# Performance work log

Hardware: AMD Instinct MI355X
Metric: run time of the kernel (lower is better)

## Reference

```python
import jax, jax.numpy as jnp
import numpy as np

GROUPS = 16
KS = 3
EPS = 1e-5  # torch InstanceNorm2d default


def _leaky(x):
    return jnp.where(x > 0, x, 0.1 * x)


def setup_inputs() -> dict:
    key = jax.random.key(0)
    ks = jax.random.split(key, 9)
    B, C, H, W = 8, 256, 128, 128
    R = 512
    s = 0.05
    return {
        "x": jax.random.normal(ks[0], (B, C, H, W), jnp.float32),
        "representation": jax.random.normal(ks[1], (B, R), jnp.float32),
        # SConv.compress_key: Linear(R, C*3*3, bias=False)
        "w_key": jax.random.normal(ks[2], (C * KS * KS, R), jnp.float32) * s,
        # SRAdaIN gamma/beta Linears (R -> C, no bias)
        "w_gamma": jax.random.normal(ks[3], (C, R), jnp.float32) * s,
        "w_beta": jax.random.normal(ks[4], (C, R), jnp.float32) * s,
        # SCM: 1x1 convs R -> R/4 -> C (no bias), PReLU single param init 0.25
        "w_ca1": jax.random.normal(ks[5], (R // 4, R), jnp.float32) * s,
        "prelu_a": jnp.float32(0.25),
        "w_ca2": jax.random.normal(ks[6], (C, R // 4), jnp.float32) * s,
        # ConvLayer: 1x1 conv C -> C with bias
        "w_conv2": jax.random.normal(ks[7], (C, C), jnp.float32) * s,
        "b_conv2": jax.random.normal(ks[8], (C,), jnp.float32) * s,
    }


def reference(x, representation, w_key, w_gamma, w_beta, w_ca1, prelu_a, w_ca2, w_conv2, b_conv2):
    b, c_in, h, w = x.shape
    c_out = w_conv2.shape[0]
    fpg = c_in // GROUPS  # features per group

    # ---- SConv: per-sample dynamic grouped conv (reflection pad, valid conv) ----
    xp = jnp.pad(x, ((0, 0), (0, 0), (1, 1), (1, 1)), mode='reflect')
    # kernel: (b, c_out, 1, 3, 3) then repeat_interleave over in-per-group dim
    kern = _leaky(representation @ w_key.T).reshape(b, c_out, 1, KS, KS)
    kern = jnp.broadcast_to(kern, (b, c_out, fpg, KS, KS))

    def one_conv(xi, ki):
        # xi: (c_in, h+2, w+2); ki: (c_out, fpg, 3, 3)
        return jax.lax.conv_general_dilated(
            xi[None], ki, (1, 1), 'VALID',
            feature_group_count=GROUPS,
            dimension_numbers=('NCHW', 'OIHW', 'NCHW'))[0]

    out = jax.vmap(one_conv)(xp, kern)  # (b, c_out, h, w)

    # ---- SRAdaIN: instance norm (biased var) + learned affine from rep ----
    mean = out.mean(axis=(2, 3), keepdims=True)
    var = out.var(axis=(2, 3), keepdims=True)
    gamma = _leaky(representation @ w_gamma.T)[:, :, None, None]
    beta = _leaky(representation @ w_beta.T)[:, :, None, None]
    out = (out - mean) * jax.lax.rsqrt(var + EPS) * gamma + beta
    out = jax.nn.relu(out)

    # ---- SCM: channel attention gating of the residual ----
    hmid = representation @ w_ca1.T
    hmid = jnp.where(hmid > 0, hmid, prelu_a * hmid)  # PReLU
    att = jax.nn.sigmoid(hmid @ w_ca2.T)[:, :, None, None]  # (b, c_out, 1, 1)
    out = out + x * att

    # ---- ConvLayer: 1x1 conv with bias (pad=0) ----
    out = jnp.einsum('bchw,oc->bohw', out, w_conv2) + b_conv2[None, :, None, None]
    return out
```

## Files before the change

### kernel.cpp

```cpp
#include <hip/hip_runtime.h>
#include <hip/hip_bf16.h>

#define NB 8
#define NC 256
#define NH 128
#define NW 128
#define NR 512
#define NGROUPS 16
#define HP 130
#define NPIX (NH*NW)

#define OFF_KERN  0
#define OFF_GAMMA 18432
#define OFF_BETA  20480
#define OFF_ATT   22528
#define OFF_A     24576
#define OFF_B2    26624
#define OFF_HMID  28672
#define OFF_P     29696
#define OFF_GP    94208
#define OFF_APACK 2257408
#define OFF_PART  2322944

typedef __attribute__((ext_vector_type(8))) short bf16x8;
typedef __attribute__((ext_vector_type(4))) float f32x4;

__device__ __forceinline__ float leakyf(float v) { return v > 0.f ? v : 0.1f * v; }

__device__ __forceinline__ unsigned short f2bf(float f) {
    unsigned u = __float_as_uint(f);
    unsigned r = (u + 0x7FFFu + ((u >> 16) & 1u)) >> 16;
    return (unsigned short)r;
}
__device__ __forceinline__ float bf2f(unsigned short s) {
    return __uint_as_float(((unsigned)s) << 16);
}

__global__ __launch_bounds__(256) void k_params(
    const float* __restrict__ rep, const float* __restrict__ w_key,
    const float* __restrict__ w_gamma, const float* __restrict__ w_beta,
    const float* __restrict__ w_ca1, const float* __restrict__ prelu_a,
    float* __restrict__ ws)
{
    __shared__ float rep_s[NR];
    const int b = blockIdx.y, t = threadIdx.x;
    rep_s[t]       = rep[b*NR + t];
    rep_s[t + 256] = rep[b*NR + t + 256];
    __syncthreads();

    const int r = blockIdx.x * 64 + (t >> 2);
    const int part = t & 3;
    const float* wrow;
    if (r < 2304)      wrow = w_key   + (size_t)r * NR;
    else if (r < 2560) wrow = w_gamma + (size_t)(r - 2304) * NR;
    else if (r < 2816) wrow = w_beta  + (size_t)(r - 2560) * NR;
    else               wrow = w_ca1   + (size_t)(r - 2816) * NR;

    const float4* w4 = (const float4*)wrow + part*32;
    const float4* r4 = (const float4*)rep_s + part*32;
    float acc = 0.f;
    #pragma unroll
    for (int i = 0; i < 32; i++) {
        float4 a = r4[i], w = w4[i];
        acc += a.x*w.x + a.y*w.y + a.z*w.z + a.w*w.w;
    }
    acc += __shfl_xor(acc, 1, 64);
    acc += __shfl_xor(acc, 2, 64);

    if (part == 0) {
        if (r < 2816) {
            const float v = leakyf(acc);
            if (r < 2304)      ws[OFF_KERN  + b*NC*9 + r]        = v;
            else if (r < 2560) ws[OFF_GAMMA + b*NC + r - 2304]   = v;
            else               ws[OFF_BETA  + b*NC + r - 2560]   = v;
        } else {
            const float pa = prelu_a[0];
            ws[OFF_HMID + b*128 + r - 2816] = acc > 0.f ? acc : pa * acc;
        }
    }
}

__global__ __launch_bounds__(256) void k_pack(
    const float* __restrict__ W, float* __restrict__ ws)
{
    const int idx = blockIdx.x * 256 + threadIdx.x;
    const int j    = idx & 7;
    const int lane = (idx >> 3) & 63;
    const int mt   = (idx >> 9) & 15;
    const int ks   = idx >> 13;
    const int m = mt*16 + (lane & 15);
    const int k = ks*32 + (lane >> 4)*8 + j;
    unsigned short* ap = (unsigned short*)(ws + OFF_APACK);
    ap[((ks*16 + mt)*64 + lane)*8 + j] = f2bf(W[m*NC + k]);
}

__global__ __launch_bounds__(256) void k_gsum(
    const float* __restrict__ x, float* __restrict__ ws)
{
    const int t = threadIdx.x;
    const int l = t & 31;
    const int r = t >> 5;
    const int bid = blockIdx.x;
    const int rg = bid % 17;
    const int bg = bid / 17;
    const int yy = rg*8 + r;
    if (yy >= HP) return;
    int sy = yy - 1; if (sy < 0) sy = -sy; if (sy > NH-1) sy = 2*(NH-1) - sy;
    const float* xbase = x + (size_t)bg * 16 * NPIX + (size_t)sy * NW + l*4;
    float4 s = make_float4(0.f, 0.f, 0.f, 0.f);
    #pragma unroll
    for (int k = 0; k < 16; k++) {
        const float4 v = *(const float4*)(xbase + (size_t)k * NPIX);
        s.x += v.x; s.y += v.y; s.z += v.z; s.w += v.w;
    }
    float* gp = ws + OFF_GP + ((size_t)bg * HP + yy) * HP;
    gp[1 + l*4] = s.x;
    gp[2 + l*4] = s.y;
    gp[3 + l*4] = s.z;
    gp[4 + l*4] = s.w;
    if (l == 0)  gp[0]   = s.y;
    if (l == 31) gp[129] = s.z;
}

__global__ __launch_bounds__(256) void k_stats(float* __restrict__ ws)
{
    const int g = blockIdx.x, b = blockIdx.y, chunk = blockIdx.z, t = threadIdx.x;
    __shared__ float kern_s[16*9];
    __shared__ float red[256*32];
    if (t < 144) kern_s[t] = ws[OFF_KERN + (b*NC + g*16)*9 + t];
    __syncthreads();

    float s[16], q[16];
    #pragma unroll
    for (int i = 0; i < 16; i++) { s[i] = 0.f; q[i] = 0.f; }

    const float* gp = ws + OFF_GP + (size_t)(b*16 + g) * HP * HP;
    const int p0b = chunk * 4096;
    for (int pi = 0; pi < 16; pi++) {
        const int p = p0b + pi*256 + t;
        const int y = p >> 7, xc = p & 127;
        const float* pa = gp + y*HP + xc;
        const float p0 = pa[0],    p1 = pa[1],      p2 = pa[2];
        const float p3 = pa[HP],   p4 = pa[HP+1],   p5 = pa[HP+2];
        const float p6 = pa[2*HP], p7 = pa[2*HP+1], p8 = pa[2*HP+2];
        #pragma unroll
        for (int ch = 0; ch < 16; ch++) {
            const float* k9 = kern_s + ch*9;
            float v = k9[0]*p0 + k9[1]*p1 + k9[2]*p2
                    + k9[3]*p3 + k9[4]*p4 + k9[5]*p5
                    + k9[6]*p6 + k9[7]*p7 + k9[8]*p8;
            s[ch] += v; q[ch] += v*v;
        }
    }
    #pragma unroll
    for (int ch = 0; ch < 16; ch++) { red[t*32 + ch] = s[ch]; red[t*32 + 16 + ch] = q[ch]; }
    for (int st = 128; st >= 1; st >>= 1) {
        __syncthreads();
        if (t < st) {
            #pragma unroll
            for (int v = 0; v < 32; v++) red[t*32 + v] += red[(t+st)*32 + v];
        }
    }
    __syncthreads();
    if (t < 32) {
        ws[OFF_PART + (size_t)((b*16 + g)*4 + chunk)*32 + t] = red[t];
    }
}

__global__ __launch_bounds__(256) void k_fin(
    const float* __restrict__ w_ca2, float* __restrict__ ws)
{
    __shared__ float hm_s[128];
    const int b = blockIdx.x, c = threadIdx.x;
    if (c < 128) hm_s[c] = ws[OFF_HMID + b*128 + c];
    float* P = ws + OFF_P + ((size_t)(b*NC + c) << 4);
    {
        const int g = c >> 4, ch = c & 15;
        const float* part = ws + OFF_PART + (size_t)(b*16 + g)*4*32;
        float S = 0.f, Q = 0.f;
        #pragma unroll
        for (int k = 0; k < 4; k++) { S += part[k*32 + ch]; Q += part[k*32 + 16 + ch]; }
        const float mean = S * (1.f/16384.f);
        const float var  = Q * (1.f/16384.f) - mean*mean;
        const float inv  = rsqrtf(var + 1e-5f);
        const float ga = ws[OFF_GAMMA + b*NC + c];
        const float be = ws[OFF_BETA  + b*NC + c];
        const float a  = ga * inv;
        #pragma unroll
        for (int k = 0; k < 9; k++) P[k] = ws[OFF_KERN + (b*NC + c)*9 + k];
        P[9]  = a;
        P[10] = be - mean * a;
    }
    __syncthreads();
    {
        const float4* w4 = (const float4*)(w_ca2 + c*128);
        const float4* h4 = (const float4*)hm_s;
        float acc = 0.f;
        #pragma unroll
        for (int i = 0; i < 32; i++) {
            float4 a = h4[i], w = w4[i];
            acc += a.x*w.x + a.y*w.y + a.z*w.z + a.w*w.w;
        }
        P[11] = 1.f / (1.f + expf(-acc));
    }
}

__global__ __launch_bounds__(256) void k_main(
    const float* __restrict__ x, const float* __restrict__ ws,
    const float* __restrict__ bias, float* __restrict__ out)
{
    __shared__ unsigned short z_t[32*256];
    __shared__ float4 P_s[NC*3];
    __shared__ float bias_s[NC];

    const int t = threadIdx.x;
    const int wave = t >> 6, lane = t & 63;
    const int x0 = blockIdx.x * 32, y = blockIdx.y, b = blockIdx.z;

    bias_s[t] = bias[t];

    {
        const float4* Pg = (const float4*)(ws + OFF_P + ((size_t)(b*NC) << 4));
        #pragma unroll
        for (int i = 0; i < 3; i++) {
            const int idx = t + i*256;
            const int c = idx / 3, k = idx - c*3;
            P_s[idx] = Pg[c*4 + k];
        }
    }

    char* zb = (char*)z_t;

    const int csub = lane >> 5;
    const int pxl  = lane & 31;
    const int cw   = wave*64 + csub*32;
    const int pxg  = x0 + pxl;
    const float* gpB = ws + OFF_GP + (size_t)b * 16 * HP * HP;
    const unsigned short* ap = (const unsigned short*)(ws + OFF_APACK);
    const float* xB = x + (size_t)(b*NC + cw) * NPIX + (size_t)y * NW + pxg;

    float xv[32];
    #pragma unroll
    for (int j = 0; j < 32; j++) xv[j] = xB[(size_t)j * NPIX];
    float pA[9], pB[9];
    {
        const float* gpr = gpB + ((size_t)(cw >> 4) * HP + y) * HP + pxg;
        #pragma unroll
        for (int k = 0; k < 9; k++) pA[k] = gpr[(k/3)*HP + (k%3)];
    }
    {
        const float* gpr = gpB + ((size_t)((cw >> 4) + 1) * HP + y) * HP + pxg;
        #pragma unroll
        for (int k = 0; k < 9; k++) pB[k] = gpr[(k/3)*HP + (k%3)];
    }
    __syncthreads();

    #pragma unroll
    for (int ii = 0; ii < 4; ii++) {
        bf16x8 zp;
        #pragma unroll
        for (int j = 0; j < 8; j++) {
            const int c = cw + ii*8 + j;
            const float4 q0 = P_s[c*3 + 0];
            const float4 q1 = P_s[c*3 + 1];
            const float4 q2 = P_s[c*3 + 2];
            const bool ub = (ii >= 2);
            const float conv =
                  (ub ? pB[0] : pA[0])*q0.x + (ub ? pB[1] : pA[1])*q0.y
                + (ub ? pB[2] : pA[2])*q0.z + (ub ? pB[3] : pA[3])*q0.w
                + (ub ? pB[4] : pA[4])*q1.x + (ub ? pB[5] : pA[5])*q1.y
                + (ub ? pB[6] : pA[6])*q1.z + (ub ? pB[7] : pA[7])*q1.w
                + (ub ? pB[8] : pA[8])*q2.x;
            const float z = fmaxf(fmaf(q2.y, conv, q2.z), 0.f) + xv[ii*8 + j] * q2.w;
            zp[j] = (short)f2bf(z);
        }
        const int c0 = cw + ii*8;
        *(bf16x8*)(zb + pxl*512 + ((c0*2) ^ ((pxl & 7) << 4))) = zp;
    }
    __syncthreads();

    f32x4 acc[4][2];
    #pragma unroll
    for (int mi = 0; mi < 4; mi++) {
        acc[mi][0] = (f32x4){0.f, 0.f, 0.f, 0.f};
        acc[mi][1] = (f32x4){0.f, 0.f, 0.f, 0.f};
    }

    #pragma unroll
    for (int ks = 0; ks < 8; ks++) {
        bf16x8 bfr[2];
        #pragma unroll
        for (int ni = 0; ni < 2; ni++) {
            const int pxc = ni*16 + (lane & 15);
            bfr[ni] = *(const bf16x8*)(zb + pxc*512 + ((ks*64 + (lane >> 4)*16) ^ ((pxc & 7) << 4)));
        }
        #pragma unroll
        for (int mi = 0; mi < 4; mi++) {
            const bf16x8 afr = *(const bf16x8*)(ap + ((size_t)((ks*16 + wave*4 + mi))*64 + lane)*8);
            #pragma unroll
            for (int ni = 0; ni < 2; ni++)
                acc[mi][ni] = __builtin_amdgcn_mfma_f32_16x16x32_bf16(afr, bfr[ni], acc[mi][ni], 0, 0, 0);
        }
    }

    #pragma unroll
    for (int mi = 0; mi < 4; mi++) {
        const int o_base = wave*64 + mi*16 + (lane >> 4)*4;
        #pragma unroll
        for (int ni = 0; ni < 2; ni++) {
            const int px = x0 + ni*16 + (lane & 15);
            #pragma unroll
            for (int r = 0; r < 4; r++) {
                const int o = o_base + r;
                out[((size_t)(b*NC + o) * NH + y) * NW + px] = acc[mi][ni][r] + bias_s[o];
            }
        }
    }
}

extern "C" void kernel_launch(void* const* d_in, const int* in_sizes, int n_in,
                              void* d_out, int out_size, void* d_ws, size_t ws_size,
                              hipStream_t stream) {
    const float* x       = (const float*)d_in[0];
    const float* rep     = (const float*)d_in[1];
    const float* w_key   = (const float*)d_in[2];
    const float* w_gamma = (const float*)d_in[3];
    const float* w_beta  = (const float*)d_in[4];
    const float* w_ca1   = (const float*)d_in[5];
    const float* prelu_a = (const float*)d_in[6];
    const float* w_ca2   = (const float*)d_in[7];
    const float* w_conv2 = (const float*)d_in[8];
    const float* b_conv2 = (const float*)d_in[9];
    float* out = (float*)d_out;
    float* ws  = (float*)d_ws;

    k_params<<<dim3(46, NB), 256, 0, stream>>>(rep, w_key, w_gamma, w_beta, w_ca1, prelu_a, ws);
    k_pack<<<256, 256, 0, stream>>>(w_conv2, ws);
    k_gsum<<<NB*NGROUPS*17, 256, 0, stream>>>(x, ws);
    k_stats<<<dim3(NGROUPS, NB, 4), 256, 0, stream>>>(ws);
    k_fin<<<NB, 256, 0, stream>>>(w_ca2, ws);
    k_main<<<dim3(4, NH, NB), 256, 0, stream>>>(x, ws, b_conv2, out);
}
```

Baseline: 130.4 us.

## Remap main-kernel threads to 4 pixels x 8 channels with vector loads

```diff
diff --git a/kernel.cpp b/kernel.cpp
--- a/kernel.cpp
+++ b/kernel.cpp
@@ -210,7 +210,7 @@
     const float* __restrict__ bias, float* __restrict__ out)
 {
     __shared__ unsigned short z_t[32*256];
-    __shared__ float4 P_s[NC*3];
+    __shared__ float4 P_s[800];
     __shared__ float bias_s[NC];
 
     const int t = threadIdx.x;
@@ -225,57 +225,62 @@
         for (int i = 0; i < 3; i++) {
             const int idx = t + i*256;
             const int c = idx / 3, k = idx - c*3;
-            P_s[idx] = Pg[c*4 + k];
+            P_s[c*3 + k + (c >> 3)] = Pg[c*4 + k];
         }
     }
 
     char* zb = (char*)z_t;
 
-    const int csub = lane >> 5;
-    const int pxl  = lane & 31;
-    const int cw   = wave*64 + csub*32;
-    const int pxg  = x0 + pxl;
+    const int pxq = lane & 7;
+    const int chs = (lane >> 3) & 7;
+    const int cw8 = wave*64 + chs*8;
+    const int g   = cw8 >> 4;
+    const int px0g = x0 + pxq*4;
     const float* gpB = ws + OFF_GP + (size_t)b * 16 * HP * HP;
     const unsigned short* ap = (const unsigned short*)(ws + OFF_APACK);
-    const float* xB = x + (size_t)(b*NC + cw) * NPIX + (size_t)y * NW + pxg;
-
-    float xv[32];
-    #pragma unroll
-    for (int j = 0; j < 32; j++) xv[j] = xB[(size_t)j * NPIX];
-    float pA[9], pB[9];
+    const float* xB = x + (size_t)(b*NC + cw8) * NPIX + (size_t)y * NW + px0g;
+
+    float gp6[3][6];
     {
-        const float* gpr = gpB + ((size_t)(cw >> 4) * HP + y) * HP + pxg;
-        #pragma unroll
-        for (int k = 0; k < 9; k++) pA[k] = gpr[(k/3)*HP + (k%3)];
-    }
-    {
-        const float* gpr = gpB + ((size_t)((cw >> 4) + 1) * HP + y) * HP + pxg;
-        #pragma unroll
-        for (int k = 0; k < 9; k++) pB[k] = gpr[(k/3)*HP + (k%3)];
-    }
-    __syncthreads();
-
-    #pragma unroll
-    for (int ii = 0; ii < 4; ii++) {
-        bf16x8 zp;
-        #pragma unroll
-        for (int j = 0; j < 8; j++) {
-            const int c = cw + ii*8 + j;
-            const float4 q0 = P_s[c*3 + 0];
-            const float4 q1 = P_s[c*3 + 1];
-            const float4 q2 = P_s[c*3 + 2];
-            const bool ub = (ii >= 2);
+        const float* gpr = gpB + ((size_t)g * HP + y) * HP + px0g;
+        #pragma unroll
+        for (int r = 0; r < 3; r++) {
+            const float2 a0 = *(const float2*)(gpr + r*HP);
+            const float2 a1 = *(const float2*)(gpr + r*HP + 2);
+            const float2 a2 = *(const float2*)(gpr + r*HP + 4);
+            gp6[r][0] = a0.x; gp6[r][1] = a0.y;
+            gp6[r][2] = a1.x; gp6[r][3] = a1.y;
+            gp6[r][4] = a2.x; gp6[r][5] = a2.y;
+        }
+    }
+    float4 xq[8];
+    #pragma unroll
+    for (int j = 0; j < 8; j++) xq[j] = *(const float4*)(xB + (size_t)j * NPIX);
+
+    __syncthreads();
+
+    bf16x8 zp[4];
+    const int base_f4 = cw8*3 + (cw8 >> 3);
+    #pragma unroll
+    for (int j = 0; j < 8; j++) {
+        const float4 q0 = P_s[base_f4 + j*3 + 0];
+        const float4 q1 = P_s[base_f4 + j*3 + 1];
+        const float4 q2 = P_s[base_f4 + j*3 + 2];
+        const float xj[4] = {xq[j].x, xq[j].y, xq[j].z, xq[j].w};
+        #pragma unroll
+        for (int i = 0; i < 4; i++) {
             const float conv =
-                  (ub ? pB[0] : pA[0])*q0.x + (ub ? pB[1] : pA[1])*q0.y
-                + (ub ? pB[2] : pA[2])*q0.z + (ub ? pB[3] : pA[3])*q0.w
-                + (ub ? pB[4] : pA[4])*q1.x + (ub ? pB[5] : pA[5])*q1.y
-                + (ub ? pB[6] : pA[6])*q1.z + (ub ? pB[7] : pA[7])*q1.w
-                + (ub ? pB[8] : pA[8])*q2.x;
-            const float z = fmaxf(fmaf(q2.y, conv, q2.z), 0.f) + xv[ii*8 + j] * q2.w;
-            zp[j] = (short)f2bf(z);
-        }
-        const int c0 = cw + ii*8;
-        *(bf16x8*)(zb + pxl*512 + ((c0*2) ^ ((pxl & 7) << 4))) = zp;
+                  gp6[0][i]*q0.x + gp6[0][i+1]*q0.y + gp6[0][i+2]*q0.z
+                + gp6[1][i]*q0.w + gp6[1][i+1]*q1.x + gp6[1][i+2]*q1.y
+                + gp6[2][i]*q1.z + gp6[2][i+1]*q1.w + gp6[2][i+2]*q2.x;
+            const float z = fmaxf(fmaf(q2.y, conv, q2.z), 0.f) + xj[i] * q2.w;
+            zp[i][j] = (short)f2bf(z);
+        }
+    }
+    #pragma unroll
+    for (int i = 0; i < 4; i++) {
+        const int px = pxq*4 + i;
+        *(bf16x8*)(zb + px*512 + ((cw8*2) ^ ((px & 31) << 4))) = zp[i];
     }
     __syncthreads();
 
@@ -292,7 +297,7 @@
         #pragma unroll
         for (int ni = 0; ni < 2; ni++) {
             const int pxc = ni*16 + (lane & 15);
-            bfr[ni] = *(const bf16x8*)(zb + pxc*512 + ((ks*64 + (lane >> 4)*16) ^ ((pxc & 7) << 4)));
+            bfr[ni] = *(const bf16x8*)(zb + pxc*512 + ((ks*64 + (lane >> 4)*16) ^ ((pxc & 31) << 4)));
         }
         #pragma unroll
         for (int mi = 0; mi < 4; mi++) {
```

After: 124.6 us. -4.4%, faster.
